# Kernel tuning notes

Hardware: AMD Instinct MI355X
Metric: run time of the kernel (lower is better)

## Reference

```python
import jax, jax.numpy as jnp
import numpy as np

B, T, J, D = 64, 800, 50, 200  # batch, context len, query len, 2*hidden

def setup_inputs() -> dict:
    key = jax.random.key(0)
    ks = jax.random.split(key, 8)
    return {
        'h':    jax.random.normal(ks[0], (B, T, D), jnp.float32),
        'u':    jax.random.normal(ks[1], (B, J, D), jnp.float32),
        'w_h':  jax.random.normal(ks[2], (D,), jnp.float32) * 0.05,
        'b_h':  jax.random.normal(ks[3], (1,), jnp.float32) * 0.05,
        'w_u':  jax.random.normal(ks[4], (D,), jnp.float32) * 0.05,
        'b_u':  jax.random.normal(ks[5], (1,), jnp.float32) * 0.05,
        'w_hu': jax.random.normal(ks[6], (D,), jnp.float32) * 0.05,
        'b_hu': jax.random.normal(ks[7], (1,), jnp.float32) * 0.05,
    }

def reference(h, u, w_h, b_h, w_u, b_u, w_hu, b_hu):
    # Similarity: s[b,t,j] = ws_h(h_t) + ws_u(u_j) + ws_hu(h_t * u_j)  (+ summed biases)
    # Computed without materializing the [B,T,J,D] expanded tensors of the original.
    sh = jnp.einsum('btd,d->bt', h, w_h)            # [B,T]
    su = jnp.einsum('bjd,d->bj', u, w_u)            # [B,J]
    shu = jnp.einsum('btd,bjd->btj', h * w_hu, u)   # [B,T,J]
    s = shu + sh[:, :, None] + su[:, None, :] + (b_h + b_u + b_hu)[0]
    # Context-to-query attention
    a = jax.nn.softmax(s, axis=2)                   # [B,T,J]
    c2q = jnp.einsum('btj,bjd->btd', a, u)          # [B,T,D]
    # Query-to-context attention
    b = jax.nn.softmax(jnp.max(s, axis=2), axis=1)  # [B,T]
    q2c = jnp.einsum('bt,btd->bd', b, h)[:, None, :]  # [B,1,D], broadcasts over T
    g = jnp.concatenate([h, c2q, h * c2q, h * q2c], axis=-1)  # [B,T,4D]
    return g
```

## Files before the change

### kernel.cpp

```cpp
#include <hip/hip_runtime.h>
#include <cstdint>
#include <cstddef>

#define B_ 64
#define T_ 800
#define J_ 50
#define D_ 200
#define TILE1 50
#define NTILE1 16
#define TT 5
#define NPASS 10

__device__ __forceinline__ float dot4(float4 a, float4 b) {
    return fmaf(a.x, b.x, fmaf(a.y, b.y, fmaf(a.z, b.z, a.w * b.w)));
}
__device__ __forceinline__ float rlane(float v, int l) {
    return __int_as_float(__builtin_amdgcn_readlane(__float_as_int(v), l));
}

__global__ __launch_bounds__(256, 4) void k1_kernel(
    const float* __restrict__ h, const float* __restrict__ u,
    const float* __restrict__ w_h, const float* __restrict__ b_h,
    const float* __restrict__ w_u, const float* __restrict__ b_u,
    const float* __restrict__ w_hu, const float* __restrict__ b_hu,
    float* __restrict__ g, float* __restrict__ smax_ws, float* __restrict__ q2c)
{
    __shared__ __align__(16) float4 uh_s[50][50];

    const int tid  = threadIdx.x;
    const int b    = blockIdx.x >> 4;
    const int tile = blockIdx.x & 15;

    if (tile == 0 && tid < D_) q2c[b * D_ + tid] = 0.f;

    for (int idx = tid; idx < 2500; idx += 256) {
        const int j = idx / 50, k = idx - (idx / 50) * 50;
        const float4 uu = *reinterpret_cast<const float4*>(&u[(b * J_ + j) * D_ + 4 * k]);
        const float4 ww = *reinterpret_cast<const float4*>(&w_hu[4 * k]);
        float4 p; p.x = uu.x * ww.x; p.y = uu.y * ww.y; p.z = uu.z * ww.z; p.w = uu.w * ww.w;
        int kk = k + ((j >> 2) & 7); if (kk >= 50) kk -= 50;
        uh_s[j][kk] = p;
    }

    const int lane = tid & 63;
    const int wfl  = __builtin_amdgcn_readfirstlane(tid >> 6);

    float4 wh_r = make_float4(0.f, 0.f, 0.f, 0.f);
    if (lane < 50) wh_r = *reinterpret_cast<const float4*>(&w_h[4 * lane]);

    float su = b_h[0] + b_u[0] + b_hu[0];
    {
        const int j = (lane < J_) ? lane : 0;
        const float* ur = u + (size_t)(b * J_ + j) * D_;
        #pragma unroll 5
        for (int k = 0; k < 50; ++k) {
            const float4 uu = *reinterpret_cast<const float4*>(&ur[4 * k]);
            su = fmaf(uu.x, w_u[4 * k + 0], su);
            su = fmaf(uu.y, w_u[4 * k + 1], su);
            su = fmaf(uu.z, w_u[4 * k + 2], su);
            su = fmaf(uu.w, w_u[4 * k + 3], su);
        }
    }
    __syncthreads();

    const int urow = (lane < 50) ? lane : 49;
    const int crot = (urow >> 2) & 7;
    const int dcol = (lane < 50) ? lane : 0;

    for (int p = wfl; p < NPASS; p += 4) {
        const int t0 = tile * TILE1 + p * TT;

        float4 h4r[TT];
        float  shr[TT];
        const float* hrow[TT];
        #pragma unroll
        for (int tt = 0; tt < TT; ++tt) {
            const int t = t0 + tt;
            hrow[tt] = h + (size_t)(b * T_ + t) * D_;
            float4 h4 = make_float4(0.f, 0.f, 0.f, 0.f);
            if (lane < 50) h4 = *reinterpret_cast<const float4*>(&hrow[tt][4 * lane]);
            h4r[tt] = h4;
            float ps = dot4(h4, wh_r);
            #pragma unroll
            for (int off = 32; off > 0; off >>= 1) ps += __shfl_xor(ps, off);
            shr[tt] = ps;
        }

        float s[TT];
        #pragma unroll
        for (int tt = 0; tt < TT; ++tt) s[tt] = su + shr[tt];
        #pragma unroll 5
        for (int k = 0; k < 50; ++k) {
            int kk = k + crot; if (kk >= 50) kk -= 50;
            const float4 uh = uh_s[urow][kk];
            #pragma unroll
            for (int tt = 0; tt < TT; ++tt) {
                const float* hr = hrow[tt];
                float acc = s[tt];
                acc = fmaf(uh.x, hr[4 * k + 0], acc);
                acc = fmaf(uh.y, hr[4 * k + 1], acc);
                acc = fmaf(uh.z, hr[4 * k + 2], acc);
                acc = fmaf(uh.w, hr[4 * k + 3], acc);
                s[tt] = acc;
            }
        }

        float a[TT];
        #pragma unroll
        for (int tt = 0; tt < TT; ++tt) {
            float m = (lane < J_) ? s[tt] : -3.4e38f;
            #pragma unroll
            for (int off = 32; off > 0; off >>= 1) m = fmaxf(m, __shfl_xor(m, off));
            float e = (lane < J_) ? __expf(s[tt] - m) : 0.f;
            float sum = e;
            #pragma unroll
            for (int off = 32; off > 0; off >>= 1) sum += __shfl_xor(sum, off);
            a[tt] = e / sum;
            if (lane == 0) smax_ws[b * T_ + (t0 + tt)] = m;
        }

        float4 c2q[TT];
        #pragma unroll
        for (int tt = 0; tt < TT; ++tt) c2q[tt] = make_float4(0.f, 0.f, 0.f, 0.f);
        const float* ub = u + (size_t)b * J_ * D_;
        #pragma unroll 2
        for (int j = 0; j < J_; ++j) {
            const float4 uc = *reinterpret_cast<const float4*>(&ub[(size_t)j * D_ + 4 * dcol]);
            #pragma unroll
            for (int tt = 0; tt < TT; ++tt) {
                const float ab = rlane(a[tt], j);
                c2q[tt].x = fmaf(ab, uc.x, c2q[tt].x);
                c2q[tt].y = fmaf(ab, uc.y, c2q[tt].y);
                c2q[tt].z = fmaf(ab, uc.z, c2q[tt].z);
                c2q[tt].w = fmaf(ab, uc.w, c2q[tt].w);
            }
        }

        #pragma unroll
        for (int tt = 0; tt < TT; ++tt) {
            const int t = t0 + tt;
            if (lane < 50) {
                const size_t go = (size_t)(b * T_ + t) * (4 * D_) + 4 * lane;
                *reinterpret_cast<float4*>(&g[go]) = h4r[tt];
                *reinterpret_cast<float4*>(&g[go + D_]) = c2q[tt];
                float4 hc;
                hc.x = h4r[tt].x * c2q[tt].x; hc.y = h4r[tt].y * c2q[tt].y;
                hc.z = h4r[tt].z * c2q[tt].z; hc.w = h4r[tt].w * c2q[tt].w;
                *reinterpret_cast<float4*>(&g[go + 2 * D_]) = hc;
            }
        }
    }
}

__global__ __launch_bounds__(256) void k3_kernel(const float* __restrict__ h,
                                                 const float* __restrict__ smax,
                                                 float* __restrict__ q2c)
{
    const int b = blockIdx.x >> 3, t8 = blockIdx.x & 7;
    const int rows0 = t8 * 100;
    const int tid = threadIdx.x, lane = tid & 63, w = tid >> 6;
    __shared__ float red[4];
    __shared__ float bs[100];

    float v[4];
    float m = -3.4e38f;
    #pragma unroll
    for (int k = 0; k < 4; ++k) {
        const int t = tid + 256 * k;
        v[k] = (t < T_) ? smax[b * T_ + t] : -3.4e38f;
        m = fmaxf(m, v[k]);
    }
    #pragma unroll
    for (int off = 32; off > 0; off >>= 1) m = fmaxf(m, __shfl_xor(m, off));
    if (lane == 0) red[w] = m;
    __syncthreads();
    m = fmaxf(fmaxf(red[0], red[1]), fmaxf(red[2], red[3]));
    __syncthreads();

    float sum = 0.f;
    #pragma unroll
    for (int k = 0; k < 4; ++k) {
        const int t = tid + 256 * k;
        sum += (t < T_) ? __expf(v[k] - m) : 0.f;
    }
    #pragma unroll
    for (int off = 32; off > 0; off >>= 1) sum += __shfl_xor(sum, off);
    if (lane == 0) red[w] = sum;
    __syncthreads();
    sum = red[0] + red[1] + red[2] + red[3];
    const float inv = 1.f / sum;

    if (tid < 100) bs[tid] = __expf(smax[b * T_ + rows0 + tid] - m) * inv;
    __syncthreads();

    if (tid < D_) {
        const float* hp = h + ((size_t)b * T_ + rows0) * D_ + tid;
        float acc = 0.f;
        #pragma unroll 10
        for (int i = 0; i < 100; ++i) acc = fmaf(bs[i], hp[(size_t)i * D_], acc);
        atomicAdd(&q2c[b * D_ + tid], acc);
    }
}

__global__ __launch_bounds__(256) void k4_kernel(const float* __restrict__ h,
                                                 const float* __restrict__ q2c,
                                                 float* __restrict__ g)
{
    const int b = blockIdx.x >> 4, tc = blockIdx.x & 15;
    const int tid = threadIdx.x;
    if (tid >= 250) return;
    const int tl = tid / 50, d4 = tid - tl * 50;
    const float4 q = *reinterpret_cast<const float4*>(&q2c[b * D_ + 4 * d4]);
    const int trow0 = tc * 50 + tl;
    #pragma unroll 5
    for (int i = 0; i < 10; ++i) {
        const int t = trow0 + 5 * i;
        const float4 h4 = *reinterpret_cast<const float4*>(&h[(size_t)(b * T_ + t) * D_ + 4 * d4]);
        float4 o;
        o.x = h4.x * q.x; o.y = h4.y * q.y; o.z = h4.z * q.z; o.w = h4.w * q.w;
        *reinterpret_cast<float4*>(&g[(size_t)(b * T_ + t) * (4 * D_) + 3 * D_ + 4 * d4]) = o;
    }
}

extern "C" void kernel_launch(void* const* d_in, const int* in_sizes, int n_in,
                              void* d_out, int out_size, void* d_ws, size_t ws_size,
                              hipStream_t stream)
{
    const float* h    = (const float*)d_in[0];
    const float* u    = (const float*)d_in[1];
    const float* w_h  = (const float*)d_in[2];
    const float* b_h  = (const float*)d_in[3];
    const float* w_u  = (const float*)d_in[4];
    const float* b_u  = (const float*)d_in[5];
    const float* w_hu = (const float*)d_in[6];
    const float* b_hu = (const float*)d_in[7];
    float* g = (float*)d_out;

    float* smax = (float*)d_ws;
    float* q2c  = smax + B_ * T_;

    k1_kernel<<<dim3(B_ * NTILE1), dim3(256), 0, stream>>>(h, u, w_h, b_h, w_u, b_u, w_hu, b_hu, g, smax, q2c);
    k3_kernel<<<dim3(B_ * 8), dim3(256), 0, stream>>>(h, smax, q2c);
    k4_kernel<<<dim3(B_ * NTILE1), dim3(256), 0, stream>>>(h, q2c, g);
}
```

Before: 304.3 us.

## Stage u and scaled h rows in LDS, use 512-thread blocks with 8 wavefronts

The similarity kernel now keeps raw u in LDS and uses it for the su dot product, the similarity inner loop, and the c2q accumulation, so repeated global/L2 reads of u and h go away. Each wavefront writes h*w_hu for its 5 rows into LDS in two halves. Softmax weights go to LDS and are read back as float4, replacing per-j readlane broadcasts. Blocks grow to 512 threads covering 100 rows each, which halves the grid and raises LDS use per block, possibly lowering occupancy. k4's grid is doubled so it keeps its previous block count.

```diff
diff --git a/kernel.cpp b/kernel.cpp
--- a/kernel.cpp
+++ b/kernel.cpp
@@ -6,80 +6,78 @@
 #define T_ 800
 #define J_ 50
 #define D_ 200
-#define TILE1 50
-#define NTILE1 16
+#define TILE1 100
+#define NTILE1 8
+#define NW 8
 #define TT 5
-#define NPASS 10
+#define NPASS 20
 
 __device__ __forceinline__ float dot4(float4 a, float4 b) {
     return fmaf(a.x, b.x, fmaf(a.y, b.y, fmaf(a.z, b.z, a.w * b.w)));
 }
-__device__ __forceinline__ float rlane(float v, int l) {
-    return __int_as_float(__builtin_amdgcn_readlane(__float_as_int(v), l));
-}
-
-__global__ __launch_bounds__(256, 4) void k1_kernel(
+__device__ __forceinline__ int rotc(int k, int j) {
+    int kk = k + ((j >> 2) & 7);
+    return (kk >= 50) ? kk - 50 : kk;
+}
+
+__global__ __launch_bounds__(512, 4) void k1_kernel(
     const float* __restrict__ h, const float* __restrict__ u,
     const float* __restrict__ w_h, const float* __restrict__ b_h,
     const float* __restrict__ w_u, const float* __restrict__ b_u,
     const float* __restrict__ w_hu, const float* __restrict__ b_hu,
     float* __restrict__ g, float* __restrict__ smax_ws, float* __restrict__ q2c)
 {
-    __shared__ __align__(16) float4 uh_s[50][50];
+    __shared__ __align__(16) float4 u4_s[50][50];
+    __shared__ __align__(16) float4 hw_s[NW][TT][25];
+    __shared__ float a_s[NW][TT][52];
 
     const int tid  = threadIdx.x;
-    const int b    = blockIdx.x >> 4;
-    const int tile = blockIdx.x & 15;
+    const int b    = blockIdx.x >> 3;
+    const int tile = blockIdx.x & 7;
 
     if (tile == 0 && tid < D_) q2c[b * D_ + tid] = 0.f;
 
-    for (int idx = tid; idx < 2500; idx += 256) {
+    for (int idx = tid; idx < 2500; idx += 512) {
         const int j = idx / 50, k = idx - (idx / 50) * 50;
-        const float4 uu = *reinterpret_cast<const float4*>(&u[(b * J_ + j) * D_ + 4 * k]);
-        const float4 ww = *reinterpret_cast<const float4*>(&w_hu[4 * k]);
-        float4 p; p.x = uu.x * ww.x; p.y = uu.y * ww.y; p.z = uu.z * ww.z; p.w = uu.w * ww.w;
-        int kk = k + ((j >> 2) & 7); if (kk >= 50) kk -= 50;
-        uh_s[j][kk] = p;
-    }
+        u4_s[j][rotc(k, j)] = *reinterpret_cast<const float4*>(&u[(b * J_ + j) * D_ + 4 * k]);
+    }
+    __syncthreads();
 
     const int lane = tid & 63;
-    const int wfl  = __builtin_amdgcn_readfirstlane(tid >> 6);
-
-    float4 wh_r = make_float4(0.f, 0.f, 0.f, 0.f);
-    if (lane < 50) wh_r = *reinterpret_cast<const float4*>(&w_h[4 * lane]);
+    const int w    = tid >> 6;
+    const int urow = (lane < 50) ? lane : 49;
+    const int dcol = (lane < 50) ? lane : 0;
+
+    float4 whu_r = make_float4(0.f, 0.f, 0.f, 0.f);
+    float4 wh_r  = make_float4(0.f, 0.f, 0.f, 0.f);
+    if (lane < 50) {
+        whu_r = *reinterpret_cast<const float4*>(&w_hu[4 * lane]);
+        wh_r  = *reinterpret_cast<const float4*>(&w_h[4 * lane]);
+    }
 
     float su = b_h[0] + b_u[0] + b_hu[0];
-    {
-        const int j = (lane < J_) ? lane : 0;
-        const float* ur = u + (size_t)(b * J_ + j) * D_;
-        #pragma unroll 5
-        for (int k = 0; k < 50; ++k) {
-            const float4 uu = *reinterpret_cast<const float4*>(&ur[4 * k]);
-            su = fmaf(uu.x, w_u[4 * k + 0], su);
-            su = fmaf(uu.y, w_u[4 * k + 1], su);
-            su = fmaf(uu.z, w_u[4 * k + 2], su);
-            su = fmaf(uu.w, w_u[4 * k + 3], su);
-        }
-    }
-    __syncthreads();
-
-    const int urow = (lane < 50) ? lane : 49;
-    const int crot = (urow >> 2) & 7;
-    const int dcol = (lane < 50) ? lane : 0;
-
-    for (int p = wfl; p < NPASS; p += 4) {
+    #pragma unroll 5
+    for (int k = 0; k < 50; ++k) {
+        const float4 wu4 = *reinterpret_cast<const float4*>(&w_u[4 * k]);
+        su += dot4(u4_s[urow][rotc(k, urow)], wu4);
+    }
+
+    for (int p = w; p < NPASS; p += NW) {
         const int t0 = tile * TILE1 + p * TT;
 
         float4 h4r[TT];
         float  shr[TT];
-        const float* hrow[TT];
-        #pragma unroll
-        for (int tt = 0; tt < TT; ++tt) {
-            const int t = t0 + tt;
-            hrow[tt] = h + (size_t)(b * T_ + t) * D_;
+        #pragma unroll
+        for (int tt = 0; tt < TT; ++tt) {
             float4 h4 = make_float4(0.f, 0.f, 0.f, 0.f);
-            if (lane < 50) h4 = *reinterpret_cast<const float4*>(&hrow[tt][4 * lane]);
+            if (lane < 50)
+                h4 = *reinterpret_cast<const float4*>(&h[(size_t)(b * T_ + t0 + tt) * D_ + 4 * lane]);
             h4r[tt] = h4;
+            if (lane < 25) {
+                float4 hw; hw.x = h4.x * whu_r.x; hw.y = h4.y * whu_r.y;
+                hw.z = h4.z * whu_r.z; hw.w = h4.w * whu_r.w;
+                hw_s[w][tt][lane] = hw;
+            }
             float ps = dot4(h4, wh_r);
             #pragma unroll
             for (int off = 32; off > 0; off >>= 1) ps += __shfl_xor(ps, off);
@@ -89,23 +87,28 @@
         float s[TT];
         #pragma unroll
         for (int tt = 0; tt < TT; ++tt) s[tt] = su + shr[tt];
+
         #pragma unroll 5
-        for (int k = 0; k < 50; ++k) {
-            int kk = k + crot; if (kk >= 50) kk -= 50;
-            const float4 uh = uh_s[urow][kk];
-            #pragma unroll
-            for (int tt = 0; tt < TT; ++tt) {
-                const float* hr = hrow[tt];
-                float acc = s[tt];
-                acc = fmaf(uh.x, hr[4 * k + 0], acc);
-                acc = fmaf(uh.y, hr[4 * k + 1], acc);
-                acc = fmaf(uh.z, hr[4 * k + 2], acc);
-                acc = fmaf(uh.w, hr[4 * k + 3], acc);
-                s[tt] = acc;
-            }
-        }
-
-        float a[TT];
+        for (int k = 0; k < 25; ++k) {
+            const float4 u4 = u4_s[urow][rotc(k, urow)];
+            #pragma unroll
+            for (int tt = 0; tt < TT; ++tt) s[tt] += dot4(hw_s[w][tt][k], u4);
+        }
+        #pragma unroll
+        for (int tt = 0; tt < TT; ++tt) {
+            if (lane >= 25 && lane < 50) {
+                float4 hw; hw.x = h4r[tt].x * whu_r.x; hw.y = h4r[tt].y * whu_r.y;
+                hw.z = h4r[tt].z * whu_r.z; hw.w = h4r[tt].w * whu_r.w;
+                hw_s[w][tt][lane - 25] = hw;
+            }
+        }
+        #pragma unroll 5
+        for (int k = 25; k < 50; ++k) {
+            const float4 u4 = u4_s[urow][rotc(k, urow)];
+            #pragma unroll
+            for (int tt = 0; tt < TT; ++tt) s[tt] += dot4(hw_s[w][tt][k - 25], u4);
+        }
+
         #pragma unroll
         for (int tt = 0; tt < TT; ++tt) {
             float m = (lane < J_) ? s[tt] : -3.4e38f;
@@ -115,32 +118,61 @@
             float sum = e;
             #pragma unroll
             for (int off = 32; off > 0; off >>= 1) sum += __shfl_xor(sum, off);
-            a[tt] = e / sum;
+            if (lane < J_) a_s[w][tt][lane] = e / sum;
             if (lane == 0) smax_ws[b * T_ + (t0 + tt)] = m;
         }
 
         float4 c2q[TT];
         #pragma unroll
         for (int tt = 0; tt < TT; ++tt) c2q[tt] = make_float4(0.f, 0.f, 0.f, 0.f);
-        const float* ub = u + (size_t)b * J_ * D_;
-        #pragma unroll 2
-        for (int j = 0; j < J_; ++j) {
-            const float4 uc = *reinterpret_cast<const float4*>(&ub[(size_t)j * D_ + 4 * dcol]);
+        #pragma unroll 3
+        for (int j4 = 0; j4 < 12; ++j4) {
+            const float4 ua0 = u4_s[4 * j4 + 0][rotc(dcol, 4 * j4 + 0)];
+            const float4 ua1 = u4_s[4 * j4 + 1][rotc(dcol, 4 * j4 + 1)];
+            const float4 ua2 = u4_s[4 * j4 + 2][rotc(dcol, 4 * j4 + 2)];
+            const float4 ua3 = u4_s[4 * j4 + 3][rotc(dcol, 4 * j4 + 3)];
             #pragma unroll
             for (int tt = 0; tt < TT; ++tt) {
-                const float ab = rlane(a[tt], j);
-                c2q[tt].x = fmaf(ab, uc.x, c2q[tt].x);
-                c2q[tt].y = fmaf(ab, uc.y, c2q[tt].y);
-                c2q[tt].z = fmaf(ab, uc.z, c2q[tt].z);
-                c2q[tt].w = fmaf(ab, uc.w, c2q[tt].w);
-            }
-        }
-
-        #pragma unroll
-        for (int tt = 0; tt < TT; ++tt) {
-            const int t = t0 + tt;
+                const float4 a4 = *reinterpret_cast<const float4*>(&a_s[w][tt][4 * j4]);
+                c2q[tt].x = fmaf(a4.x, ua0.x, c2q[tt].x);
+                c2q[tt].y = fmaf(a4.x, ua0.y, c2q[tt].y);
+                c2q[tt].z = fmaf(a4.x, ua0.z, c2q[tt].z);
+                c2q[tt].w = fmaf(a4.x, ua0.w, c2q[tt].w);
+                c2q[tt].x = fmaf(a4.y, ua1.x, c2q[tt].x);
+                c2q[tt].y = fmaf(a4.y, ua1.y, c2q[tt].y);
+                c2q[tt].z = fmaf(a4.y, ua1.z, c2q[tt].z);
+                c2q[tt].w = fmaf(a4.y, ua1.w, c2q[tt].w);
+                c2q[tt].x = fmaf(a4.z, ua2.x, c2q[tt].x);
+                c2q[tt].y = fmaf(a4.z, ua2.y, c2q[tt].y);
+                c2q[tt].z = fmaf(a4.z, ua2.z, c2q[tt].z);
+                c2q[tt].w = fmaf(a4.z, ua2.w, c2q[tt].w);
+                c2q[tt].x = fmaf(a4.w, ua3.x, c2q[tt].x);
+                c2q[tt].y = fmaf(a4.w, ua3.y, c2q[tt].y);
+                c2q[tt].z = fmaf(a4.w, ua3.z, c2q[tt].z);
+                c2q[tt].w = fmaf(a4.w, ua3.w, c2q[tt].w);
+            }
+        }
+        {
+            const float4 ua0 = u4_s[48][rotc(dcol, 48)];
+            const float4 ua1 = u4_s[49][rotc(dcol, 49)];
+            #pragma unroll
+            for (int tt = 0; tt < TT; ++tt) {
+                const float a0 = a_s[w][tt][48], a1 = a_s[w][tt][49];
+                c2q[tt].x = fmaf(a0, ua0.x, c2q[tt].x);
+                c2q[tt].y = fmaf(a0, ua0.y, c2q[tt].y);
+                c2q[tt].z = fmaf(a0, ua0.z, c2q[tt].z);
+                c2q[tt].w = fmaf(a0, ua0.w, c2q[tt].w);
+                c2q[tt].x = fmaf(a1, ua1.x, c2q[tt].x);
+                c2q[tt].y = fmaf(a1, ua1.y, c2q[tt].y);
+                c2q[tt].z = fmaf(a1, ua1.z, c2q[tt].z);
+                c2q[tt].w = fmaf(a1, ua1.w, c2q[tt].w);
+            }
+        }
+
+        #pragma unroll
+        for (int tt = 0; tt < TT; ++tt) {
             if (lane < 50) {
-                const size_t go = (size_t)(b * T_ + t) * (4 * D_) + 4 * lane;
+                const size_t go = (size_t)(b * T_ + t0 + tt) * (4 * D_) + 4 * lane;
                 *reinterpret_cast<float4*>(&g[go]) = h4r[tt];
                 *reinterpret_cast<float4*>(&g[go + D_]) = c2q[tt];
                 float4 hc;
@@ -239,7 +271,7 @@
     float* smax = (float*)d_ws;
     float* q2c  = smax + B_ * T_;
 
-    k1_kernel<<<dim3(B_ * NTILE1), dim3(256), 0, stream>>>(h, u, w_h, b_h, w_u, b_u, w_hu, b_hu, g, smax, q2c);
+    k1_kernel<<<dim3(B_ * NTILE1), dim3(512), 0, stream>>>(h, u, w_h, b_h, w_u, b_u, w_hu, b_hu, g, smax, q2c);
     k3_kernel<<<dim3(B_ * 8), dim3(256), 0, stream>>>(h, smax, q2c);
-    k4_kernel<<<dim3(B_ * NTILE1), dim3(256), 0, stream>>>(h, q2c, g);
-}
+    k4_kernel<<<dim3(B_ * NTILE1 * 2), dim3(256), 0, stream>>>(h, q2c, g);
+}
```

New measurement: 276.8 us. 9.0% less time.
